# Kernel optimization log

Hardware: AMD Instinct MI355X
Metric: run time of the kernel (lower is better)

## Reference

```python
import jax, jax.numpy as jnp
import numpy as np

B, IN, H = 4096, 1024, 1024


def setup_inputs() -> dict:
    key = jax.random.key(0)
    ks = jax.random.split(key, 16)
    s = 1.0 / np.sqrt(IN)
    inp = {
        "x_t": jax.random.normal(ks[0], (B, IN), jnp.float32),
        "h_prev": jax.random.normal(ks[1], (B, H), jnp.float32),
        "c_prev": jax.random.normal(ks[2], (B, H), jnp.float32),
        "W_xi": jax.random.uniform(ks[3], (H, IN), jnp.float32, -s, s),
        "W_hi": jax.random.normal(ks[4], (H, H), jnp.float32) / np.sqrt(H),
        "b_i": jnp.zeros((H,), jnp.float32),
        "W_xf": jax.random.uniform(ks[5], (H, IN), jnp.float32, -s, s),
        "W_hf": jax.random.normal(ks[6], (H, H), jnp.float32) / np.sqrt(H),
        "b_f": jnp.ones((H,), jnp.float32),
        "W_xg": jax.random.uniform(ks[7], (H, IN), jnp.float32, -s, s),
        "W_hg": jax.random.normal(ks[8], (H, H), jnp.float32) / np.sqrt(H),
        "b_g": jnp.zeros((H,), jnp.float32),
        "W_xo": jax.random.uniform(ks[9], (H, IN), jnp.float32, -s, s),
        "W_ho": jax.random.normal(ks[10], (H, H), jnp.float32) / np.sqrt(H),
        "b_o": jnp.zeros((H,), jnp.float32),
    }
    return inp


def reference(x_t, h_prev, c_prev,
              W_xi, W_hi, b_i,
              W_xf, W_hf, b_f,
              W_xg, W_hg, b_g,
              W_xo, W_ho, b_o):
    # i/f/g/o gates: sigmoid/sigmoid/tanh/sigmoid of (x W_x^T + h W_h^T + b)
    i_t = jax.nn.sigmoid(x_t @ W_xi.T + h_prev @ W_hi.T + b_i)
    f_t = jax.nn.sigmoid(x_t @ W_xf.T + h_prev @ W_hf.T + b_f)
    g_t = jnp.tanh(x_t @ W_xg.T + h_prev @ W_hg.T + b_g)
    o_t = jax.nn.sigmoid(x_t @ W_xo.T + h_prev @ W_ho.T + b_o)
    c_t = f_t * c_prev + i_t * g_t
    h_t = o_t * jnp.tanh(c_t)
    return (h_t, c_t)
```

## Files before the change

### kernel.cpp

```cpp
#include <hip/hip_runtime.h>
#include <hip/hip_bf16.h>


constexpr int Mdim = 4096;
constexpr int Ndim = 4096;
constexpr int Kdim = 2048;
constexpr int Hdim = 1024;
constexpr int BM = 256;
constexpr int BN = 256;
constexpr int BK = 64;
constexpr int NT = Kdim / BK;

using short8 = __attribute__((ext_vector_type(8))) short;
using f32x4  = __attribute__((ext_vector_type(4))) float;

__device__ __forceinline__ float sigmoid_(float x) {
    return 1.f / (1.f + __expf(-x));
}
__device__ __forceinline__ float tanh_(float x) {
    float e = __expf(2.f * x);
    return (e - 1.f) / (e + 1.f);
}

__global__ void build_A(const float* __restrict__ x, const float* __restrict__ h,
                        __hip_bfloat16* __restrict__ A) {
    int idx = blockIdx.x * 256 + threadIdx.x;
    int row = idx >> 8;
    int c8  = (idx & 255) * 8;
    const float* src = (c8 < 1024) ? (x + (size_t)row * 1024 + c8)
                                   : (h + (size_t)row * 1024 + (c8 - 1024));
    float4 f0 = ((const float4*)src)[0];
    float4 f1 = ((const float4*)src)[1];
    union { short8 v; __hip_bfloat16 e[8]; } u;
    u.e[0] = __float2bfloat16(f0.x); u.e[1] = __float2bfloat16(f0.y);
    u.e[2] = __float2bfloat16(f0.z); u.e[3] = __float2bfloat16(f0.w);
    u.e[4] = __float2bfloat16(f1.x); u.e[5] = __float2bfloat16(f1.y);
    u.e[6] = __float2bfloat16(f1.z); u.e[7] = __float2bfloat16(f1.w);
    *(short8*)(A + (size_t)row * Kdim + c8) = u.v;
}

__global__ void build_B(const float* __restrict__ Wxi, const float* __restrict__ Whi,
                        const float* __restrict__ Wxf, const float* __restrict__ Whf,
                        const float* __restrict__ Wxg, const float* __restrict__ Whg,
                        const float* __restrict__ Wxo, const float* __restrict__ Who,
                        __hip_bfloat16* __restrict__ B) {
    int idx = blockIdx.x * 256 + threadIdx.x;
    int n  = idx >> 8;
    int c8 = (idx & 255) * 8;
    int g = (n >> 4) & 3;
    int j = ((n >> 6) << 4) | (n & 15);
    const float* Wx = (g == 0) ? Wxi : (g == 1) ? Wxf : (g == 2) ? Wxg : Wxo;
    const float* Wh = (g == 0) ? Whi : (g == 1) ? Whf : (g == 2) ? Whg : Who;
    const float* src = (c8 < 1024) ? (Wx + (size_t)j * 1024 + c8)
                                   : (Wh + (size_t)j * 1024 + (c8 - 1024));
    float4 f0 = ((const float4*)src)[0];
    float4 f1 = ((const float4*)src)[1];
    union { short8 v; __hip_bfloat16 e[8]; } u;
    u.e[0] = __float2bfloat16(f0.x); u.e[1] = __float2bfloat16(f0.y);
    u.e[2] = __float2bfloat16(f0.z); u.e[3] = __float2bfloat16(f0.w);
    u.e[4] = __float2bfloat16(f1.x); u.e[5] = __float2bfloat16(f1.y);
    u.e[6] = __float2bfloat16(f1.z); u.e[7] = __float2bfloat16(f1.w);
    *(short8*)(B + (size_t)n * Kdim + c8) = u.v;
}

#define BAR() __builtin_amdgcn_s_barrier()

__launch_bounds__(512, 1)
__global__ void lstm_gemm(const __hip_bfloat16* __restrict__ A,
                          const __hip_bfloat16* __restrict__ B,
                          const float* __restrict__ c_prev,
                          const float* __restrict__ b_i, const float* __restrict__ b_f,
                          const float* __restrict__ b_g, const float* __restrict__ b_o,
                          float* __restrict__ out_h, float* __restrict__ out_c) {
    __shared__ __hip_bfloat16 lds[2][2][2][256 * 32];

    const int tid  = threadIdx.x;
    const int lane = tid & 63;
    const int w    = tid >> 6;
    const int wr   = w >> 2;
    const int wc   = w & 3;
    const int l15  = lane & 15, lhi = lane >> 4;

    int bid = blockIdx.x;
    int swz = (bid & 7) * 32 + (bid >> 3);
    const int bm = (swz >> 4) * BM;
    const int bn = (swz & 15) * BN;

    const int srow  = tid >> 2;
    const int scole = (((tid & 3) * 16) ^ (((tid >> 2) & 6) << 3)) >> 1;

    const int koff = (lhi * 16) ^ ((l15 & 6) << 3);

#define STG(dstbase, srcptr, growbase, kcol)                                    \
    do {                                                                        \
        _Pragma("unroll")                                                       \
        for (int i_ = 0; i_ < 2; ++i_)                                          \
            __builtin_amdgcn_global_load_lds(                                   \
                (const __attribute__((address_space(1))) unsigned*)(            \
                    (srcptr) + (size_t)((growbase) + i_ * 128 + srow) * Kdim    \
                    + (kcol) + scole),                                          \
                (__attribute__((address_space(3))) unsigned*)(                  \
                    (char*)(dstbase) + i_ * 8192 + tid * 16), 16, 0, 0);        \
    } while (0)

#define RDA(d, kk, a) (*(const short8*)((const char*)&lds[d][0][kk][0] + \
                        (wr * 128 + (a) * 16 + l15) * 64 + koff))
#define RDB(d, kk, b) (*(const short8*)((const char*)&lds[d][1][kk][0] + \
                        (wc * 64 + (b) * 16 + l15) * 64 + koff))

    f32x4 acc[8][4];
#pragma unroll
    for (int a = 0; a < 8; ++a)
#pragma unroll
        for (int b = 0; b < 4; ++b)
            acc[a][b] = (f32x4){0.f, 0.f, 0.f, 0.f};

    STG(&lds[0][0][0][0], A, bm, 0);
    STG(&lds[0][1][0][0], B, bn, 0);
    STG(&lds[0][0][1][0], A, bm, 32);
    STG(&lds[0][1][1][0], B, bn, 32);
    STG(&lds[1][0][0][0], A, bm, 64);
    STG(&lds[1][1][0][0], B, bn, 64);
    asm volatile("s_waitcnt vmcnt(4)" ::: "memory");
    BAR();

    for (int t = 0; t < NT; ++t) {
        const int d = t & 1;

        short8 af0 = RDA(d, 0, 0), af1 = RDA(d, 0, 1), af2 = RDA(d, 0, 2), af3 = RDA(d, 0, 3);
        short8 bf0[4];
#pragma unroll
        for (int b = 0; b < 4; ++b) bf0[b] = RDB(d, 0, b);
        if (t + 1 < NT) {
            STG(&lds[d ^ 1][0][1][0], A, bm, (t + 1) * BK + 32);
            STG(&lds[d ^ 1][1][1][0], B, bn, (t + 1) * BK + 32);
        }
        BAR();
        __builtin_amdgcn_s_setprio(1);
#pragma unroll
        for (int b = 0; b < 4; ++b) {
            acc[0][b] = __builtin_amdgcn_mfma_f32_16x16x32_bf16(af0, bf0[b], acc[0][b], 0, 0, 0);
            acc[1][b] = __builtin_amdgcn_mfma_f32_16x16x32_bf16(af1, bf0[b], acc[1][b], 0, 0, 0);
            acc[2][b] = __builtin_amdgcn_mfma_f32_16x16x32_bf16(af2, bf0[b], acc[2][b], 0, 0, 0);
            acc[3][b] = __builtin_amdgcn_mfma_f32_16x16x32_bf16(af3, bf0[b], acc[3][b], 0, 0, 0);
        }
        __builtin_amdgcn_s_setprio(0);
        BAR();

        short8 af4 = RDA(d, 0, 4), af5 = RDA(d, 0, 5), af6 = RDA(d, 0, 6), af7 = RDA(d, 0, 7);
        BAR();
        __builtin_amdgcn_s_setprio(1);
#pragma unroll
        for (int b = 0; b < 4; ++b) {
            acc[4][b] = __builtin_amdgcn_mfma_f32_16x16x32_bf16(af4, bf0[b], acc[4][b], 0, 0, 0);
            acc[5][b] = __builtin_amdgcn_mfma_f32_16x16x32_bf16(af5, bf0[b], acc[5][b], 0, 0, 0);
            acc[6][b] = __builtin_amdgcn_mfma_f32_16x16x32_bf16(af6, bf0[b], acc[6][b], 0, 0, 0);
            acc[7][b] = __builtin_amdgcn_mfma_f32_16x16x32_bf16(af7, bf0[b], acc[7][b], 0, 0, 0);
        }
        __builtin_amdgcn_s_setprio(0);
        BAR();

        af0 = RDA(d, 1, 0); af1 = RDA(d, 1, 1); af2 = RDA(d, 1, 2); af3 = RDA(d, 1, 3);
        short8 bf1[4];
#pragma unroll
        for (int b = 0; b < 4; ++b) bf1[b] = RDB(d, 1, b);
        if (t + 2 < NT)
            STG(&lds[d][0][0][0], A, bm, (t + 2) * BK);
        BAR();
        __builtin_amdgcn_s_setprio(1);
#pragma unroll
        for (int b = 0; b < 4; ++b) {
            acc[0][b] = __builtin_amdgcn_mfma_f32_16x16x32_bf16(af0, bf1[b], acc[0][b], 0, 0, 0);
            acc[1][b] = __builtin_amdgcn_mfma_f32_16x16x32_bf16(af1, bf1[b], acc[1][b], 0, 0, 0);
            acc[2][b] = __builtin_amdgcn_mfma_f32_16x16x32_bf16(af2, bf1[b], acc[2][b], 0, 0, 0);
            acc[3][b] = __builtin_amdgcn_mfma_f32_16x16x32_bf16(af3, bf1[b], acc[3][b], 0, 0, 0);
        }
        __builtin_amdgcn_s_setprio(0);
        BAR();

        af4 = RDA(d, 1, 4); af5 = RDA(d, 1, 5); af6 = RDA(d, 1, 6); af7 = RDA(d, 1, 7);
        if (t + 2 < NT)
            STG(&lds[d][1][0][0], B, bn, (t + 2) * BK);
        BAR();
        __builtin_amdgcn_s_setprio(1);
#pragma unroll
        for (int b = 0; b < 4; ++b) {
            acc[4][b] = __builtin_amdgcn_mfma_f32_16x16x32_bf16(af4, bf1[b], acc[4][b], 0, 0, 0);
            acc[5][b] = __builtin_amdgcn_mfma_f32_16x16x32_bf16(af5, bf1[b], acc[5][b], 0, 0, 0);
            acc[6][b] = __builtin_amdgcn_mfma_f32_16x16x32_bf16(af6, bf1[b], acc[6][b], 0, 0, 0);
            acc[7][b] = __builtin_amdgcn_mfma_f32_16x16x32_bf16(af7, bf1[b], acc[7][b], 0, 0, 0);
        }
        __builtin_amdgcn_s_setprio(0);
        if (t < NT - 2)       asm volatile("s_waitcnt vmcnt(4)" ::: "memory");
        else if (t == NT - 2) asm volatile("s_waitcnt vmcnt(0)" ::: "memory");
        BAR();
    }
#undef STG
#undef RDA
#undef RDB

    const int j0 = ((bn + wc * 64) >> 6) * 16 + l15;
    const float bi  = b_i[j0];
    const float bf_ = b_f[j0];
    const float bg  = b_g[j0];
    const float bo  = b_o[j0];

#pragma unroll
    for (int a = 0; a < 8; ++a) {
        int mbase = bm + wr * 128 + a * 16 + lhi * 4;
#pragma unroll
        for (int r = 0; r < 4; ++r) {
            int m = mbase + r;
            float vi = acc[a][0][r] + bi;
            float vf = acc[a][1][r] + bf_;
            float vg = acc[a][2][r] + bg;
            float vo = acc[a][3][r] + bo;
            float it = sigmoid_(vi);
            float ft = sigmoid_(vf);
            float gt = tanh_(vg);
            float ot = sigmoid_(vo);
            float cp = c_prev[(size_t)m * Hdim + j0];
            float ct = ft * cp + it * gt;
            float ht = ot * tanh_(ct);
            out_h[(size_t)m * Hdim + j0] = ht;
            out_c[(size_t)m * Hdim + j0] = ct;
        }
    }
}

extern "C" void kernel_launch(void* const* d_in, const int* in_sizes, int n_in,
                              void* d_out, int out_size, void* d_ws, size_t ws_size,
                              hipStream_t stream) {
    const float* x_t    = (const float*)d_in[0];
    const float* h_prev = (const float*)d_in[1];
    const float* c_prev = (const float*)d_in[2];
    const float* W_xi   = (const float*)d_in[3];
    const float* W_hi   = (const float*)d_in[4];
    const float* b_i    = (const float*)d_in[5];
    const float* W_xf   = (const float*)d_in[6];
    const float* W_hf   = (const float*)d_in[7];
    const float* b_f    = (const float*)d_in[8];
    const float* W_xg   = (const float*)d_in[9];
    const float* W_hg   = (const float*)d_in[10];
    const float* b_g    = (const float*)d_in[11];
    const float* W_xo   = (const float*)d_in[12];
    const float* W_ho   = (const float*)d_in[13];
    const float* b_o    = (const float*)d_in[14];

    float* out_h = (float*)d_out;
    float* out_c = out_h + (size_t)Mdim * Hdim;

    __hip_bfloat16* Abf = (__hip_bfloat16*)d_ws;
    __hip_bfloat16* Bbf = Abf + (size_t)Mdim * Kdim;

    build_A<<<4096, 256, 0, stream>>>(x_t, h_prev, Abf);
    build_B<<<4096, 256, 0, stream>>>(W_xi, W_hi, W_xf, W_hf, W_xg, W_hg, W_xo, W_ho, Bbf);

    lstm_gemm<<<dim3((Mdim / BM) * (Ndim / BN)), 512, 0, stream>>>(
        Abf, Bbf, c_prev, b_i, b_f, b_g, b_o, out_h, out_c);
}
```

Measured before the change: 90.20 us.

## Restructure LDS layout to 128x64 halves with quadrant-ordered MFMA pipeline

Reorganizes shared memory into 128-row by 64-wide-K slabs with an XOR swizzle on 16-byte chunks, and reads both K halves per fragment at once. The main loop is reordered into four quadrant phases that reuse A and B fragments across quadrants, interleaving the next tile's global-to-LDS loads between phases with adjusted vmcnt waits. It also raises launch bounds to allow two blocks per CU. The intent is fewer LDS reads per MFMA and better overlap of loads with compute. The cost is more register pressure, and possible spills under the two-block bound.

```diff
diff --git a/kernel.cpp b/kernel.cpp
--- a/kernel.cpp
+++ b/kernel.cpp
@@ -64,15 +64,16 @@
 }
 
 #define BAR() __builtin_amdgcn_s_barrier()
-
-__launch_bounds__(512, 1)
+#define RD(p) (*(const short8*)(p))
+
+__launch_bounds__(512, 2)
 __global__ void lstm_gemm(const __hip_bfloat16* __restrict__ A,
                           const __hip_bfloat16* __restrict__ B,
                           const float* __restrict__ c_prev,
                           const float* __restrict__ b_i, const float* __restrict__ b_f,
                           const float* __restrict__ b_g, const float* __restrict__ b_o,
                           float* __restrict__ out_h, float* __restrict__ out_c) {
-    __shared__ __hip_bfloat16 lds[2][2][2][256 * 32];
+    __shared__ __hip_bfloat16 lds[2][2][2][128 * 64];
 
     const int tid  = threadIdx.x;
     const int lane = tid & 63;
@@ -86,27 +87,19 @@
     const int bm = (swz >> 4) * BM;
     const int bn = (swz & 15) * BN;
 
-    const int srow  = tid >> 2;
-    const int scole = (((tid & 3) * 16) ^ (((tid >> 2) & 6) << 3)) >> 1;
-
-    const int koff = (lhi * 16) ^ ((l15 & 6) << 3);
-
-#define STG(dstbase, srcptr, growbase, kcol)                                    \
-    do {                                                                        \
-        _Pragma("unroll")                                                       \
-        for (int i_ = 0; i_ < 2; ++i_)                                          \
-            __builtin_amdgcn_global_load_lds(                                   \
-                (const __attribute__((address_space(1))) unsigned*)(            \
-                    (srcptr) + (size_t)((growbase) + i_ * 128 + srow) * Kdim    \
-                    + (kcol) + scole),                                          \
-                (__attribute__((address_space(3))) unsigned*)(                  \
-                    (char*)(dstbase) + i_ * 8192 + tid * 16), 16, 0, 0);        \
-    } while (0)
-
-#define RDA(d, kk, a) (*(const short8*)((const char*)&lds[d][0][kk][0] + \
-                        (wr * 128 + (a) * 16 + l15) * 64 + koff))
-#define RDB(d, kk, b) (*(const short8*)((const char*)&lds[d][1][kk][0] + \
-                        (wc * 64 + (b) * 16 + l15) * 64 + koff))
+    const int srow_  = tid >> 3;
+    const int schunk = ((tid & 7) ^ ((tid >> 3) & 7)) * 8;
+
+    const int swz4 = (l15 & 7) << 4;
+    const int kof0 = (lhi * 16) ^ swz4;
+    const int kof1 = (64 + lhi * 16) ^ swz4;
+
+#define STG1(dstbase, byteoff, srcptr, grow, kcol)                              \
+    __builtin_amdgcn_global_load_lds(                                           \
+        (const __attribute__((address_space(1))) unsigned*)(                    \
+            (srcptr) + (size_t)((grow) + srow_) * Kdim + (kcol) + schunk),      \
+        (__attribute__((address_space(3))) unsigned*)(                          \
+            (char*)(dstbase) + (byteoff) + tid * 16), 16, 0, 0)
 
     f32x4 acc[8][4];
 #pragma unroll
@@ -115,89 +108,115 @@
         for (int b = 0; b < 4; ++b)
             acc[a][b] = (f32x4){0.f, 0.f, 0.f, 0.f};
 
-    STG(&lds[0][0][0][0], A, bm, 0);
-    STG(&lds[0][1][0][0], B, bn, 0);
-    STG(&lds[0][0][1][0], A, bm, 32);
-    STG(&lds[0][1][1][0], B, bn, 32);
-    STG(&lds[1][0][0][0], A, bm, 64);
-    STG(&lds[1][1][0][0], B, bn, 64);
-    asm volatile("s_waitcnt vmcnt(4)" ::: "memory");
+    STG1(&lds[0][1][0][0], 0,    B, bn + 0,   0);
+    STG1(&lds[0][1][0][0], 8192, B, bn + 64,  0);
+    STG1(&lds[0][1][1][0], 0,    B, bn + 128, 0);
+    STG1(&lds[0][1][1][0], 8192, B, bn + 192, 0);
+    STG1(&lds[0][0][0][0], 0,    A, bm + 0,   0);
+    STG1(&lds[0][0][1][0], 0,    A, bm + 128, 0);
+    STG1(&lds[0][0][0][0], 8192, A, bm + 64,  0);
+    STG1(&lds[0][0][1][0], 8192, A, bm + 192, 0);
+    asm volatile("s_waitcnt vmcnt(0)" ::: "memory");
     BAR();
 
     for (int t = 0; t < NT; ++t) {
-        const int d = t & 1;
-
-        short8 af0 = RDA(d, 0, 0), af1 = RDA(d, 0, 1), af2 = RDA(d, 0, 2), af3 = RDA(d, 0, 3);
-        short8 bf0[4];
-#pragma unroll
-        for (int b = 0; b < 4; ++b) bf0[b] = RDB(d, 0, b);
-        if (t + 1 < NT) {
-            STG(&lds[d ^ 1][0][1][0], A, bm, (t + 1) * BK + 32);
-            STG(&lds[d ^ 1][1][1][0], B, bn, (t + 1) * BK + 32);
-        }
-        BAR();
-        __builtin_amdgcn_s_setprio(1);
-#pragma unroll
-        for (int b = 0; b < 4; ++b) {
-            acc[0][b] = __builtin_amdgcn_mfma_f32_16x16x32_bf16(af0, bf0[b], acc[0][b], 0, 0, 0);
-            acc[1][b] = __builtin_amdgcn_mfma_f32_16x16x32_bf16(af1, bf0[b], acc[1][b], 0, 0, 0);
-            acc[2][b] = __builtin_amdgcn_mfma_f32_16x16x32_bf16(af2, bf0[b], acc[2][b], 0, 0, 0);
-            acc[3][b] = __builtin_amdgcn_mfma_f32_16x16x32_bf16(af3, bf0[b], acc[3][b], 0, 0, 0);
-        }
-        __builtin_amdgcn_s_setprio(0);
-        BAR();
-
-        short8 af4 = RDA(d, 0, 4), af5 = RDA(d, 0, 5), af6 = RDA(d, 0, 6), af7 = RDA(d, 0, 7);
-        BAR();
-        __builtin_amdgcn_s_setprio(1);
-#pragma unroll
-        for (int b = 0; b < 4; ++b) {
-            acc[4][b] = __builtin_amdgcn_mfma_f32_16x16x32_bf16(af4, bf0[b], acc[4][b], 0, 0, 0);
-            acc[5][b] = __builtin_amdgcn_mfma_f32_16x16x32_bf16(af5, bf0[b], acc[5][b], 0, 0, 0);
-            acc[6][b] = __builtin_amdgcn_mfma_f32_16x16x32_bf16(af6, bf0[b], acc[6][b], 0, 0, 0);
-            acc[7][b] = __builtin_amdgcn_mfma_f32_16x16x32_bf16(af7, bf0[b], acc[7][b], 0, 0, 0);
-        }
-        __builtin_amdgcn_s_setprio(0);
-        BAR();
-
-        af0 = RDA(d, 1, 0); af1 = RDA(d, 1, 1); af2 = RDA(d, 1, 2); af3 = RDA(d, 1, 3);
-        short8 bf1[4];
-#pragma unroll
-        for (int b = 0; b < 4; ++b) bf1[b] = RDB(d, 1, b);
-        if (t + 2 < NT)
-            STG(&lds[d][0][0][0], A, bm, (t + 2) * BK);
-        BAR();
-        __builtin_amdgcn_s_setprio(1);
-#pragma unroll
-        for (int b = 0; b < 4; ++b) {
-            acc[0][b] = __builtin_amdgcn_mfma_f32_16x16x32_bf16(af0, bf1[b], acc[0][b], 0, 0, 0);
-            acc[1][b] = __builtin_amdgcn_mfma_f32_16x16x32_bf16(af1, bf1[b], acc[1][b], 0, 0, 0);
-            acc[2][b] = __builtin_amdgcn_mfma_f32_16x16x32_bf16(af2, bf1[b], acc[2][b], 0, 0, 0);
-            acc[3][b] = __builtin_amdgcn_mfma_f32_16x16x32_bf16(af3, bf1[b], acc[3][b], 0, 0, 0);
-        }
-        __builtin_amdgcn_s_setprio(0);
-        BAR();
-
-        af4 = RDA(d, 1, 4); af5 = RDA(d, 1, 5); af6 = RDA(d, 1, 6); af7 = RDA(d, 1, 7);
-        if (t + 2 < NT)
-            STG(&lds[d][1][0][0], B, bn, (t + 2) * BK);
-        BAR();
-        __builtin_amdgcn_s_setprio(1);
-#pragma unroll
-        for (int b = 0; b < 4; ++b) {
-            acc[4][b] = __builtin_amdgcn_mfma_f32_16x16x32_bf16(af4, bf1[b], acc[4][b], 0, 0, 0);
-            acc[5][b] = __builtin_amdgcn_mfma_f32_16x16x32_bf16(af5, bf1[b], acc[5][b], 0, 0, 0);
-            acc[6][b] = __builtin_amdgcn_mfma_f32_16x16x32_bf16(af6, bf1[b], acc[6][b], 0, 0, 0);
-            acc[7][b] = __builtin_amdgcn_mfma_f32_16x16x32_bf16(af7, bf1[b], acc[7][b], 0, 0, 0);
-        }
-        __builtin_amdgcn_s_setprio(0);
-        if (t < NT - 2)       asm volatile("s_waitcnt vmcnt(4)" ::: "memory");
-        else if (t == NT - 2) asm volatile("s_waitcnt vmcnt(0)" ::: "memory");
+        const int d  = t & 1;
+        const int kn = (t + 1) * BK;
+        const char* Ab = (const char*)&lds[d][0][wr][0] + l15 * 128;
+        const char* Bb = (const char*)&lds[d][1][wc >> 1][0] + ((wc & 1) * 64 + l15) * 128;
+
+        short8 af[4][2];
+        short8 bf01[2][2];
+        short8 bf23[2][2];
+
+#pragma unroll
+        for (int a = 0; a < 4; ++a) {
+            af[a][0] = RD(Ab + a * 2048 + kof0);
+            af[a][1] = RD(Ab + a * 2048 + kof1);
+        }
+#pragma unroll
+        for (int b = 0; b < 2; ++b) {
+            bf01[b][0] = RD(Bb + b * 2048 + kof0);
+            bf01[b][1] = RD(Bb + b * 2048 + kof1);
+        }
+        if (t + 1 < NT) {
+            STG1(&lds[d ^ 1][1][0][0], 0,    B, bn + 0,  kn);
+            STG1(&lds[d ^ 1][1][0][0], 8192, B, bn + 64, kn);
+        }
+        BAR();
+        __builtin_amdgcn_s_setprio(1);
+#pragma unroll
+        for (int a = 0; a < 4; ++a)
+#pragma unroll
+            for (int b = 0; b < 2; ++b)
+#pragma unroll
+                for (int kk = 0; kk < 2; ++kk)
+                    acc[a][b] = __builtin_amdgcn_mfma_f32_16x16x32_bf16(af[a][kk], bf01[b][kk], acc[a][b], 0, 0, 0);
+        __builtin_amdgcn_s_setprio(0);
+        BAR();
+
+#pragma unroll
+        for (int b = 0; b < 2; ++b) {
+            bf23[b][0] = RD(Bb + (2 + b) * 2048 + kof0);
+            bf23[b][1] = RD(Bb + (2 + b) * 2048 + kof1);
+        }
+        if (t + 1 < NT) {
+            STG1(&lds[d ^ 1][1][1][0], 0,    B, bn + 128, kn);
+            STG1(&lds[d ^ 1][1][1][0], 8192, B, bn + 192, kn);
+        }
+        BAR();
+        __builtin_amdgcn_s_setprio(1);
+#pragma unroll
+        for (int a = 0; a < 4; ++a)
+#pragma unroll
+            for (int b = 0; b < 2; ++b)
+#pragma unroll
+                for (int kk = 0; kk < 2; ++kk)
+                    acc[a][2 + b] = __builtin_amdgcn_mfma_f32_16x16x32_bf16(af[a][kk], bf23[b][kk], acc[a][2 + b], 0, 0, 0);
+        __builtin_amdgcn_s_setprio(0);
+        if (t < NT - 1) asm volatile("s_waitcnt vmcnt(4)" ::: "memory");
+        else            asm volatile("s_waitcnt vmcnt(0)" ::: "memory");
+        BAR();
+
+#pragma unroll
+        for (int a = 0; a < 4; ++a) {
+            af[a][0] = RD(Ab + (4 + a) * 2048 + kof0);
+            af[a][1] = RD(Ab + (4 + a) * 2048 + kof1);
+        }
+        if (t + 1 < NT) {
+            STG1(&lds[d ^ 1][0][0][0], 0, A, bm + 0,   kn);
+            STG1(&lds[d ^ 1][0][1][0], 0, A, bm + 128, kn);
+        }
+        BAR();
+        __builtin_amdgcn_s_setprio(1);
+#pragma unroll
+        for (int a = 0; a < 4; ++a)
+#pragma unroll
+            for (int b = 0; b < 2; ++b)
+#pragma unroll
+                for (int kk = 0; kk < 2; ++kk)
+                    acc[4 + a][2 + b] = __builtin_amdgcn_mfma_f32_16x16x32_bf16(af[a][kk], bf23[b][kk], acc[4 + a][2 + b], 0, 0, 0);
+        __builtin_amdgcn_s_setprio(0);
+        BAR();
+
+        if (t + 1 < NT) {
+            STG1(&lds[d ^ 1][0][0][0], 8192, A, bm + 64,  kn);
+            STG1(&lds[d ^ 1][0][1][0], 8192, A, bm + 192, kn);
+        }
+        BAR();
+        __builtin_amdgcn_s_setprio(1);
+#pragma unroll
+        for (int a = 0; a < 4; ++a)
+#pragma unroll
+            for (int b = 0; b < 2; ++b)
+#pragma unroll
+                for (int kk = 0; kk < 2; ++kk)
+                    acc[4 + a][b] = __builtin_amdgcn_mfma_f32_16x16x32_bf16(af[a][kk], bf01[b][kk], acc[4 + a][b], 0, 0, 0);
+        __builtin_amdgcn_s_setprio(0);
+        if (t < NT - 1) asm volatile("s_waitcnt vmcnt(2)" ::: "memory");
         BAR();
     }
-#undef STG
-#undef RDA
-#undef RDB
+#undef STG1
 
     const int j0 = ((bn + wc * 64) >> 6) * 16 + l15;
     const float bi  = b_i[j0];
```

New measurement: 86.09 us. -4.6%, faster.
